# Optimization experiments

Measured on AMD Instinct MI355X. Metric: run time of the kernel, lower is better.

## Reference

```python
import jax, jax.numpy as jnp
import numpy as np

B, S, E = 2, 2048, 2048
H, G = 32, 8          # n_heads, n_groups
D = E // H            # head_dim = 64


def setup_inputs() -> dict:
    key = jax.random.key(0)
    ks = jax.random.split(key, 5)
    scale = 1.0 / np.sqrt(E)
    return {
        "X": jax.random.normal(ks[0], (B, S, E), dtype=jnp.float32),
        "Wq": jax.random.normal(ks[1], (E, E), dtype=jnp.float32) * scale,
        "Wk": jax.random.normal(ks[2], (E, G * D), dtype=jnp.float32) * scale,
        "Wv": jax.random.normal(ks[3], (E, G * D), dtype=jnp.float32) * scale,
        "Wo": jax.random.normal(ks[4], (E, E), dtype=jnp.float32) * scale,
    }


def reference(X, Wq, Wk, Wv, Wo):
    b, s, e = X.shape
    # projections
    q = (X @ Wq).reshape(b, s, H, D).transpose(0, 2, 1, 3)      # [B,H,S,D]
    k = (X @ Wk).reshape(b, s, G, D).transpose(0, 2, 1, 3)      # [B,G,S,D]
    v = (X @ Wv).reshape(b, s, G, D).transpose(0, 2, 1, 3)      # [B,G,S,D]
    # torch view(B, H//G, G, S, D): head h -> (a=h//G, g=h%G)
    q = q.reshape(b, H // G, G, s, D)                           # [B,A,G,S,D]
    scores = jnp.einsum('bagsd,bgtd->bagst', q, k) / np.sqrt(D) # [B,A,G,S,S]
    causal = jnp.tril(jnp.ones((s, s), dtype=bool))
    scores = jnp.where(causal, scores, -jnp.inf)
    probs = jax.nn.softmax(scores, axis=-1)
    out = jnp.einsum('bagst,bgtd->bagsd', probs, v)             # [B,A,G,S,D]
    out = out.reshape(b, H, s, D).transpose(0, 2, 1, 3).reshape(b, s, e)
    return out @ Wo
```

## Files before the change

### kernel.cpp

```cpp
#include <hip/hip_runtime.h>
#include <hip/hip_bf16.h>

typedef unsigned short u16;
typedef __bf16 bf16x8 __attribute__((ext_vector_type(8)));
typedef float f32x4 __attribute__((ext_vector_type(4)));
typedef unsigned short u16x4 __attribute__((ext_vector_type(4)));

#define MFMA16(a, b, c) __builtin_amdgcn_mfma_f32_16x16x32_bf16(a, b, c, 0, 0, 0)

__device__ __forceinline__ u16 f2bf(float f) {
  union { float f; unsigned u; } v; v.f = f;
  unsigned r = v.u + 0x7FFFu + ((v.u >> 16) & 1u);
  return (u16)(r >> 16);
}

__device__ __forceinline__ u16 f2bf_native(float f) {
  __hip_bfloat16 hb = __float2bfloat16(f);
  u16 out;
  __builtin_memcpy(&out, &hb, 2);
  return out;
}

__device__ __forceinline__ void gload16(const u16* g, u16* l) {
  __builtin_amdgcn_global_load_lds(
      (const __attribute__((address_space(1))) unsigned int*)g,
      (__attribute__((address_space(3))) unsigned int*)l, 16, 0, 0);
}

__global__ void cvt_x(const float* __restrict__ X, u16* __restrict__ Xb, int n4) {
  int i = blockIdx.x * blockDim.x + threadIdx.x;
  if (i < n4) {
    float4 v = ((const float4*)X)[i];
    u16x4 o = { f2bf(v.x), f2bf(v.y), f2bf(v.z), f2bf(v.w) };
    ((u16x4*)Xb)[i] = o;
  }
}

__global__ void transpose_cvt(const float* __restrict__ W, u16* __restrict__ WT, int K, int N) {
  __shared__ float t[32][33];
  int n0 = blockIdx.x * 32, k0 = blockIdx.y * 32;
  int tx = threadIdx.x, ty = threadIdx.y;
  t[ty][tx] = W[(size_t)(k0 + ty) * N + n0 + tx];
  __syncthreads();
  WT[(size_t)(n0 + ty) * K + k0 + tx] = f2bf(t[tx][ty]);
}

template <int STORE>
__global__ __launch_bounds__(256) void gemm_bt(const u16* __restrict__ A,
                                               const u16* __restrict__ BT,
                                               void* __restrict__ Cv,
                                               int M, int N, int K) {
  __shared__ u16 lA[128 * 32];
  __shared__ u16 lB[128 * 32];
  const int tid = threadIdx.x;
  const int lane = tid & 63;
  const int wave = tid >> 6;
  const int wm = (wave >> 1) * 64, wn = (wave & 1) * 64;
  const int bm = blockIdx.y * 128, bn = blockIdx.x * 128;
  const int l15 = lane & 15, l4 = lane >> 4;

  f32x4 acc[4][4] = {};

  for (int k0 = 0; k0 < K; k0 += 32) {
    __syncthreads();
#pragma unroll
    for (int it = 0; it < 2; ++it) {
      int s = it * 256 + tid;
      int row = s >> 2, pkb = s & 3;
      int kb = pkb ^ ((row >> 1) & 3);
      gload16(A + (size_t)(bm + row) * K + k0 + kb * 8, &lA[s * 8]);
      gload16(BT + (size_t)(bn + row) * K + k0 + kb * 8, &lB[s * 8]);
    }
    __syncthreads();
    bf16x8 af[4], bf[4];
#pragma unroll
    for (int i = 0; i < 4; ++i) {
      int r = wm + i * 16 + l15;
      int pk = l4 ^ ((r >> 1) & 3);
      af[i] = *(const bf16x8*)&lA[r * 32 + pk * 8];
      int n = wn + i * 16 + l15;
      int pkn = l4 ^ ((n >> 1) & 3);
      bf[i] = *(const bf16x8*)&lB[n * 32 + pkn * 8];
    }
#pragma unroll
    for (int i = 0; i < 4; ++i)
#pragma unroll
      for (int j = 0; j < 4; ++j)
        acc[i][j] = MFMA16(af[i], bf[j], acc[i][j]);
  }

#pragma unroll
  for (int i = 0; i < 4; ++i) {
    int row = bm + wm + i * 16 + l4 * 4;
#pragma unroll
    for (int j = 0; j < 4; ++j) {
      int col = bn + wn + j * 16 + l15;
#pragma unroll
      for (int e = 0; e < 4; ++e) {
        float v = acc[i][j][e];
        if (STORE == 2) {
          ((float*)Cv)[(size_t)(row + e) * N + col] = v;
        } else {
          u16* Qb = (u16*)Cv;
          u16* Kb = Qb + 8388608;
          u16* Vt = Kb + 2097152;
          if (col < 2048)       Qb[(size_t)(row + e) * 2048 + col] = f2bf(v * 0.125f);
          else if (col < 2560)  Kb[(size_t)(row + e) * 512 + (col - 2048)] = f2bf(v);
          else                  Vt[(size_t)(col - 2560) * 4096 + (row + e)] = f2bf(v);
        }
      }
    }
  }
}

__global__ __launch_bounds__(512) void attn_fwd(const u16* __restrict__ Q,
                                                const u16* __restrict__ Kb,
                                                const u16* __restrict__ VT,
                                                u16* __restrict__ AO) {
  const int pair = blockIdx.x, g = blockIdx.y, b = blockIdx.z;
  const int tid = threadIdx.x;
  const int lane = tid & 63;
  const int wave = tid >> 6;
  const int a = wave >> 1;
  const int h = a * 8 + g;
  const int l15 = lane & 15, l4 = lane >> 4;

  __shared__ u16 Klds[2][64 * 64];
  __shared__ u16 Vlds[2][64 * 64];
  __shared__ u16 Plds[8][16 * 64];

  const int srow = tid >> 3, sc = (tid & 7) ^ (srow & 7);

  int cur = 0;
#pragma unroll 1
  for (int pass = 0; pass < 2; ++pass) {
    const int qt = (pass == 0) ? pair : 63 - pair;
    const int qw0 = qt * 32 + (wave & 1) * 16;
    const int nt = qt / 2 + 1;

    const u16* qp = Q + (size_t)(b * 2048 + qw0 + l15) * 2048 + h * 64 + l4 * 8;
    bf16x8 qf0 = *(const bf16x8*)qp;
    bf16x8 qf1 = *(const bf16x8*)(qp + 32);

    float m_r = -1e30f, l_r = 0.f;
    f32x4 o[4] = {};

    {
      gload16(Kb + (size_t)(b * 2048 + 0 + srow) * 512 + g * 64 + sc * 8, &Klds[cur][tid * 8]);
      gload16(VT + (size_t)(g * 64 + srow) * 4096 + b * 2048 + 0 + sc * 8, &Vlds[cur][tid * 8]);
      asm volatile("s_waitcnt vmcnt(0)" ::: "memory");
      __builtin_amdgcn_s_barrier();
    }

#pragma unroll 1
    for (int ti = 0; ti < nt; ++ti) {
      const int t0 = ti * 64;
      if (ti + 1 < nt) {
        const int tn = t0 + 64;
        gload16(Kb + (size_t)(b * 2048 + tn + srow) * 512 + g * 64 + sc * 8, &Klds[cur ^ 1][tid * 8]);
        gload16(VT + (size_t)(g * 64 + srow) * 4096 + b * 2048 + tn + sc * 8, &Vlds[cur ^ 1][tid * 8]);
      }

      if (t0 <= qw0 + 15) {
        const u16* Kc = Klds[cur];
        const u16* Vc = Vlds[cur];
        f32x4 s[4];
        __builtin_amdgcn_s_setprio(1);
#pragma unroll
        for (int ct = 0; ct < 4; ++ct) {
          int t = ct * 16 + l15;
          bf16x8 kf0 = *(const bf16x8*)&Kc[(t * 8 + (l4 ^ (t & 7))) * 8];
          bf16x8 kf1 = *(const bf16x8*)&Kc[(t * 8 + ((l4 + 4) ^ (t & 7))) * 8];
          f32x4 sv = {0.f, 0.f, 0.f, 0.f};
          sv = MFMA16(kf0, qf0, sv);
          sv = MFMA16(kf1, qf1, sv);
          s[ct] = sv;
        }
        __builtin_amdgcn_s_setprio(0);

        if (t0 + 63 > qw0) {
          const int qg = qw0 + l15;
#pragma unroll
          for (int ct = 0; ct < 4; ++ct)
#pragma unroll
            for (int e = 0; e < 4; ++e) {
              int tg = t0 + ct * 16 + l4 * 4 + e;
              if (tg > qg) s[ct][e] = -1e30f;
            }
        }

        float m0 = fmaxf(fmaxf(s[0][0], s[0][1]), fmaxf(s[0][2], s[0][3]));
        float m1 = fmaxf(fmaxf(s[1][0], s[1][1]), fmaxf(s[1][2], s[1][3]));
        float m2 = fmaxf(fmaxf(s[2][0], s[2][1]), fmaxf(s[2][2], s[2][3]));
        float m3 = fmaxf(fmaxf(s[3][0], s[3][1]), fmaxf(s[3][2], s[3][3]));
        float mt = fmaxf(fmaxf(m0, m1), fmaxf(m2, m3));
        mt = fmaxf(mt, __shfl_xor(mt, 16));
        mt = fmaxf(mt, __shfl_xor(mt, 32));

        if (!__all(mt <= m_r + 8.0f)) {
          float mn = fmaxf(m_r, mt);
          float alpha = __expf(m_r - mn);
          m_r = mn;
          l_r *= alpha;
#pragma unroll
          for (int e = 0; e < 4; ++e) {
            float ae = __shfl(alpha, l4 * 4 + e);
            o[0][e] *= ae; o[1][e] *= ae; o[2][e] *= ae; o[3][e] *= ae;
          }
        }

        u16* P = Plds[wave];
        float rs = 0.f;
#pragma unroll
        for (int ct = 0; ct < 4; ++ct) {
          u16x4 pk;
#pragma unroll
          for (int e = 0; e < 4; ++e) {
            float p = __expf(s[ct][e] - m_r);
            rs += p;
            pk[e] = f2bf_native(p);
          }
          int slot = (ct * 2 + (l4 >> 1)) ^ (l15 & 7);
          *(u16x4*)&P[l15 * 64 + slot * 8 + (l4 & 1) * 4] = pk;
        }
        rs += __shfl_xor(rs, 16);
        rs += __shfl_xor(rs, 32);
        l_r += rs;

        __builtin_amdgcn_s_setprio(1);
#pragma unroll
        for (int kk = 0; kk < 2; ++kk) {
          bf16x8 pf = *(const bf16x8*)&P[l15 * 64 + (((kk * 4 + l4) ^ (l15 & 7)) * 8)];
#pragma unroll
          for (int cd = 0; cd < 4; ++cd) {
            int d = cd * 16 + l15;
            bf16x8 vf = *(const bf16x8*)&Vc[(d * 8 + ((kk * 4 + l4) ^ (d & 7))) * 8];
            o[cd] = MFMA16(pf, vf, o[cd]);
          }
        }
        __builtin_amdgcn_s_setprio(0);
      }

      asm volatile("s_waitcnt vmcnt(0)" ::: "memory");
      __builtin_amdgcn_s_barrier();
      cur ^= 1;
    }

    float rli = 1.0f / l_r;
#pragma unroll
    for (int cd = 0; cd < 4; ++cd)
#pragma unroll
      for (int e = 0; e < 4; ++e) {
        float rle = __shfl(rli, l4 * 4 + e);
        int r = l4 * 4 + e;
        int d = cd * 16 + l15;
        AO[(size_t)(b * 2048 + qw0 + r) * 2048 + h * 64 + d] = f2bf_native(o[cd][e] * rle);
      }
  }
}

extern "C" void kernel_launch(void* const* d_in, const int* in_sizes, int n_in,
                              void* d_out, int out_size, void* d_ws, size_t ws_size,
                              hipStream_t stream) {
  const float* X  = (const float*)d_in[0];
  const float* Wq = (const float*)d_in[1];
  const float* Wk = (const float*)d_in[2];
  const float* Wv = (const float*)d_in[3];
  const float* Wo = (const float*)d_in[4];
  float* out = (float*)d_out;

  u16* ws  = (u16*)d_ws;
  u16* Xb  = ws;
  u16* WqT = Xb  + 8388608;
  u16* WkT = WqT + 4194304;
  u16* WvT = WkT + 1048576;
  u16* WoT = WvT + 1048576;
  u16* Qb  = WoT + 4194304;
  u16* Kbf = Qb  + 8388608;
  u16* VTb = Kbf + 2097152;
  u16* AOb = Xb;

  cvt_x<<<8192, 256, 0, stream>>>(X, Xb, 2097152);
  dim3 tb(32, 32);
  transpose_cvt<<<dim3(64, 64), tb, 0, stream>>>(Wq, WqT, 2048, 2048);
  transpose_cvt<<<dim3(16, 64), tb, 0, stream>>>(Wk, WkT, 2048, 512);
  transpose_cvt<<<dim3(16, 64), tb, 0, stream>>>(Wv, WvT, 2048, 512);
  transpose_cvt<<<dim3(64, 64), tb, 0, stream>>>(Wo, WoT, 2048, 2048);

  gemm_bt<4><<<dim3(24, 32), 256, 0, stream>>>(Xb, WqT, Qb, 4096, 3072, 2048);

  attn_fwd<<<dim3(32, 8, 2), 512, 0, stream>>>(Qb, Kbf, VTb, AOb);

  gemm_bt<2><<<dim3(16, 32), 256, 0, stream>>>(AOb, WoT, out, 4096, 2048, 2048);
}
```

Measured before the change: 230.4 us.

## Double-buffer GEMM LDS tiles with 512-thread 128x256 blocks and swizzled block order

Replaces the 256-thread 128x128 GEMM with a 512-thread kernel computing 128x256 tiles. The LDS tiles are double-buffered so the next K-slice is prefetched while MFMAs run on the current one, which cuts the loop to one barrier per iteration. Block IDs are remapped to improve L2 reuse, and MFMA sections run at raised wave priority. The cost is double the LDS footprint and larger blocks, which may reduce occupancy; the grid also shrinks to 384 and 256 blocks.

```diff
diff --git a/kernel.cpp b/kernel.cpp
--- a/kernel.cpp
+++ b/kernel.cpp
@@ -45,48 +45,72 @@
   WT[(size_t)(n0 + ty) * K + k0 + tx] = f2bf(t[tx][ty]);
 }
 
+__device__ __forceinline__ void stage_tile(const u16* __restrict__ A, const u16* __restrict__ BT,
+                                           u16* la, u16* lb, int bm, int bn, int K, int k0, int tid) {
+  {
+    int arow = tid >> 2;
+    int ac = (tid & 3) ^ ((arow >> 1) & 3);
+    gload16(A + (size_t)(bm + arow) * K + k0 + ac * 8, la + tid * 8);
+  }
+#pragma unroll
+  for (int i = 0; i < 2; ++i) {
+    int s = i * 512 + tid;
+    int brow = s >> 2;
+    int bc = (s & 3) ^ ((brow >> 1) & 3);
+    gload16(BT + (size_t)(bn + brow) * K + k0 + bc * 8, lb + s * 8);
+  }
+}
+
 template <int STORE>
-__global__ __launch_bounds__(256) void gemm_bt(const u16* __restrict__ A,
-                                               const u16* __restrict__ BT,
-                                               void* __restrict__ Cv,
-                                               int M, int N, int K) {
-  __shared__ u16 lA[128 * 32];
-  __shared__ u16 lB[128 * 32];
+__global__ __launch_bounds__(512) void gemm8(const u16* __restrict__ A,
+                                             const u16* __restrict__ BT,
+                                             void* __restrict__ Cv,
+                                             int M, int N, int K) {
+  __shared__ u16 lA[2][128 * 32];
+  __shared__ u16 lB[2][256 * 32];
   const int tid = threadIdx.x;
-  const int lane = tid & 63;
-  const int wave = tid >> 6;
-  const int wm = (wave >> 1) * 64, wn = (wave & 1) * 64;
-  const int bm = blockIdx.y * 128, bn = blockIdx.x * 128;
+  const int lane = tid & 63, wave = tid >> 6;
+  const int gx = gridDim.x;
+  const int nwg = gx * gridDim.y;
+  const int bid = blockIdx.y * gx + blockIdx.x;
+  const int sw = (bid & 7) * (nwg >> 3) + (bid >> 3);
+  const int bx = sw % gx, by = sw / gx;
+  const int bm = by * 128, bn = bx * 256;
+  const int wm = (wave >> 2) * 64, wn = (wave & 3) * 64;
   const int l15 = lane & 15, l4 = lane >> 4;
 
   f32x4 acc[4][4] = {};
 
-  for (int k0 = 0; k0 < K; k0 += 32) {
-    __syncthreads();
-#pragma unroll
-    for (int it = 0; it < 2; ++it) {
-      int s = it * 256 + tid;
-      int row = s >> 2, pkb = s & 3;
-      int kb = pkb ^ ((row >> 1) & 3);
-      gload16(A + (size_t)(bm + row) * K + k0 + kb * 8, &lA[s * 8]);
-      gload16(BT + (size_t)(bn + row) * K + k0 + kb * 8, &lB[s * 8]);
-    }
-    __syncthreads();
+  u16* ra = (u16*)lA[0]; u16* rb = (u16*)lB[0];
+  u16* wa = (u16*)lA[1]; u16* wb = (u16*)lB[1];
+
+  stage_tile(A, BT, ra, rb, bm, bn, K, 0, tid);
+  asm volatile("s_waitcnt vmcnt(0)" ::: "memory");
+  __builtin_amdgcn_s_barrier();
+
+  const int NT = K >> 5;
+#pragma unroll 1
+  for (int t = 0; t < NT; ++t) {
+    if (t + 1 < NT) stage_tile(A, BT, wa, wb, bm, bn, K, (t + 1) << 5, tid);
     bf16x8 af[4], bf[4];
 #pragma unroll
     for (int i = 0; i < 4; ++i) {
       int r = wm + i * 16 + l15;
-      int pk = l4 ^ ((r >> 1) & 3);
-      af[i] = *(const bf16x8*)&lA[r * 32 + pk * 8];
+      af[i] = *(const bf16x8*)&ra[r * 32 + (l4 ^ ((r >> 1) & 3)) * 8];
       int n = wn + i * 16 + l15;
-      int pkn = l4 ^ ((n >> 1) & 3);
-      bf[i] = *(const bf16x8*)&lB[n * 32 + pkn * 8];
+      bf[i] = *(const bf16x8*)&rb[n * 32 + (l4 ^ ((n >> 1) & 3)) * 8];
     }
+    __builtin_amdgcn_s_setprio(1);
 #pragma unroll
     for (int i = 0; i < 4; ++i)
 #pragma unroll
       for (int j = 0; j < 4; ++j)
         acc[i][j] = MFMA16(af[i], bf[j], acc[i][j]);
+    __builtin_amdgcn_s_setprio(0);
+    asm volatile("s_waitcnt vmcnt(0)" ::: "memory");
+    __builtin_amdgcn_s_barrier();
+    u16* t1 = ra; ra = wa; wa = t1;
+    u16* t2 = rb; rb = wb; wb = t2;
   }
 
 #pragma unroll
@@ -287,9 +311,9 @@
   transpose_cvt<<<dim3(16, 64), tb, 0, stream>>>(Wv, WvT, 2048, 512);
   transpose_cvt<<<dim3(64, 64), tb, 0, stream>>>(Wo, WoT, 2048, 2048);
 
-  gemm_bt<4><<<dim3(24, 32), 256, 0, stream>>>(Xb, WqT, Qb, 4096, 3072, 2048);
+  gemm8<4><<<dim3(12, 32), 512, 0, stream>>>(Xb, WqT, Qb, 4096, 3072, 2048);
 
   attn_fwd<<<dim3(32, 8, 2), 512, 0, stream>>>(Qb, Kbf, VTb, AOb);
 
-  gemm_bt<2><<<dim3(16, 32), 256, 0, stream>>>(AOb, WoT, out, 4096, 2048, 2048);
-}
+  gemm8<2><<<dim3(8, 32), 512, 0, stream>>>(AOb, WoT, out, 4096, 2048, 2048);
+}
```

Result: faster. 225.5 us (-2.1%).
